# Kernel optimization log

Hardware: AMD Instinct MI355X
Metric: run time of the kernel (lower is better)

The kernel has to match this reference:

```python
import jax, jax.numpy as jnp
import numpy as np

L = 256            # model length (match states)
Q = 2 * L + 3      # num_states = 2*length + 3
M = 1              # num_models
B = 256            # batch of sequences
T = 512            # sequence length (timesteps)
EPS = 1e-16


def setup_inputs() -> dict:
    key = jax.random.key(0)
    k1, k2, k3 = jax.random.split(key, 3)
    return {
        "emission_probs": jax.random.uniform(k1, (T, M, B, Q), dtype=jnp.float32),
        "log_A": jax.random.normal(k2, (M, Q, Q), dtype=jnp.float32),
        "init_logits": jax.random.normal(k3, (M, Q), dtype=jnp.float32),
    }


def reference(emission_probs, log_A, init_logits):
    # Dense transition matrix per model (row-stochastic), as in transitioner.make_log_A()
    A = jax.nn.softmax(log_A, axis=-1)                 # (M, Q, Q)
    init_dist = jax.nn.softmax(init_logits, axis=-1)   # (M, Q)

    def norm_step(E, R, ll):
        # One scaled-forward update: multiply emission, normalize, accumulate loglik.
        E = jnp.maximum(E, EPS)
        R = jnp.maximum(R, EPS)
        a = E * R                                      # (M, B, Q)
        S = jnp.sum(a, axis=-1, keepdims=True)         # (M, B, 1)
        ll = ll + jnp.log(S)
        a = a / S
        return a, ll

    # t = 0: init=True -> R is the initial distribution (no transition applied)
    R0 = jnp.broadcast_to(init_dist[:, None, :], (M, B, Q))
    fwd0, ll0 = norm_step(emission_probs[0], R0, jnp.zeros((M, B, 1), jnp.float32))
    out0 = jnp.concatenate([jnp.log(fwd0), ll0], axis=-1)  # (M, B, Q+1)

    def step(carry, E_t):
        fwd, ll = carry
        # transitioner(old_scaled_forward): dense transition matvec per model
        R = jnp.einsum('mbq,mqk->mbk', fwd, A)
        a, ll = norm_step(E_t, R, ll)
        return (a, ll), jnp.concatenate([jnp.log(a), ll], axis=-1)

    _, outs = jax.lax.scan(step, (fwd0, ll0), emission_probs[1:])
    outs = jnp.concatenate([out0[None], outs], axis=0)     # (T, M, B, Q+1)
    # RNN output layout: (M*B, T, Q+1)
    return jnp.transpose(outs, (1, 2, 0, 3)).reshape(M * B, T, Q + 1)
```

## Files before the change

kernel.cpp:

```cpp
#include <hip/hip_runtime.h>
#include <cstdint>

typedef unsigned u32t;
typedef unsigned long long u64;
typedef float f32x4 __attribute__((ext_vector_type(4)));
typedef short s16x4 __attribute__((ext_vector_type(4)));

#define Qn   515
#define QP   520
#define Bn   256
#define Tn   512
#define OQ   516
#define EPSc 1e-16f
#define NSL  65
#define NT   5
#define KT   33
#define KTA  17
#define USTR 532
#define NGRP 32
#define NBLK 8
#define RWORDS 264

#define WS_AMATH 0
#define WS_INIT  565760
#define WS_PAY   568320
#define WS_FLG   (WS_PAY + 540672)
#define WS_TOTAL (WS_FLG + 32768)

#define L_FRAG 0
#define L_UST  (NT*KT*64*8)
#define L_USL  (L_UST + 16*USTR*2)
#define L_SIG  (L_USL + 8*68*4)
#define LDS_TOTAL (L_SIG + 128)

__device__ __forceinline__ unsigned bfbits(float x) {
    unsigned u = __builtin_bit_cast(unsigned, x);
    unsigned r = u + 0x7FFFu + ((u >> 16) & 1u);
    return r >> 16;
}
__device__ __forceinline__ float bflo(u32t w) {
    return __builtin_bit_cast(float, w << 16);
}
__device__ __forceinline__ float bfhi(u32t w) {
    return __builtin_bit_cast(float, w & 0xffff0000u);
}

__global__ void prep_A(const float* __restrict__ logA, unsigned* __restrict__ AMATh) {
    __shared__ float red[4];
    __shared__ float srow[Qn];
    int row = blockIdx.x, tid = threadIdx.x;
    if (row >= Qn) {
        for (int c = tid; c < 260; c += 256) AMATh[(size_t)row*260 + c] = 0u;
        return;
    }
    float mx = -1e30f;
    for (int c = tid; c < Qn; c += 256) { float x = logA[(size_t)row*Qn + c]; srow[c] = x; mx = fmaxf(mx, x); }
#pragma unroll
    for (int o = 32; o > 0; o >>= 1) mx = fmaxf(mx, __shfl_xor(mx, o));
    if ((tid & 63) == 0) red[tid >> 6] = mx;
    __syncthreads();
    mx = fmaxf(fmaxf(red[0], red[1]), fmaxf(red[2], red[3]));
    __syncthreads();
    float sm = 0.f;
    for (int c = tid; c < Qn; c += 256) sm += __expf(srow[c] - mx);
#pragma unroll
    for (int o = 32; o > 0; o >>= 1) sm += __shfl_xor(sm, o);
    if ((tid & 63) == 0) red[tid >> 6] = sm;
    __syncthreads();
    float inv = 1.f / (red[0] + red[1] + red[2] + red[3]);
    for (int c2 = tid; c2 < 260; c2 += 256) {
        int c = 2*c2;
        float v0 = (c   < Qn) ? __expf(srow[c]   - mx) * inv : 0.f;
        float v1 = (c+1 < Qn) ? __expf(srow[c+1] - mx) * inv : 0.f;
        AMATh[(size_t)row*260 + c2] = bfbits(v0) | (bfbits(v1) << 16);
    }
}

__global__ void prep_init(const float* __restrict__ il, float* __restrict__ INITD) {
    __shared__ float red[4];
    __shared__ float srow[Qn];
    int tid = threadIdx.x;
    float mx = -1e30f;
    for (int c = tid; c < Qn; c += 256) { float x = il[c]; srow[c] = x; mx = fmaxf(mx, x); }
#pragma unroll
    for (int o = 32; o > 0; o >>= 1) mx = fmaxf(mx, __shfl_xor(mx, o));
    if ((tid & 63) == 0) red[tid >> 6] = mx;
    __syncthreads();
    mx = fmaxf(fmaxf(red[0], red[1]), fmaxf(red[2], red[3]));
    __syncthreads();
    float sm = 0.f;
    for (int c = tid; c < Qn; c += 256) sm += __expf(srow[c] - mx);
#pragma unroll
    for (int o = 32; o > 0; o >>= 1) sm += __shfl_xor(sm, o);
    if ((tid & 63) == 0) red[tid >> 6] = sm;
    __syncthreads();
    float inv = 1.f / (red[0] + red[1] + red[2] + red[3]);
    for (int c = tid; c < 520; c += 256)
        INITD[c] = (c < Qn) ? __expf(srow[c] - mx) * inv : 0.f;
}

__global__ void __launch_bounds__(256, 1)
hmm_fwd(const float* __restrict__ E, const unsigned* __restrict__ AMATh,
        const float* __restrict__ INITD, float* __restrict__ out,
        u32t* __restrict__ pay, u32t* __restrict__ flg)
{
    extern __shared__ char smem[];
    uint2* frag = (uint2*)(smem + L_FRAG);
    unsigned short* ustage = (unsigned short*)(smem + L_UST);
    u32t* ustage32 = (u32t*)ustage;
    float* usl  = (float*)(smem + L_USL);
    float* invs = (float*)(smem + L_SIG);
    float* lsig = invs + 8;

    const int tid  = threadIdx.x;
    const int lane = tid & 63;
    const int wv   = tid >> 6;
    const int bid  = blockIdx.x;
    const int g    = bid & 31;
    const int j    = bid >> 5;
    const int b0   = g * 8;
    const int q0   = j * NSL;

    for (int f = tid; f < NT*KT*64; f += 256) {
        int tile = f >> 6, l = f & 63;
        int nt = tile / KT, kt = tile - nt*KT;
        int col = q0 + nt*16 + (l & 15);
        int kb  = kt*16 + ((l >> 4) << 2);
        unsigned h[4];
#pragma unroll
        for (int i = 0; i < 4; ++i) {
            int pk_ = kb + i;
            int jr = pk_ / 66, rr = pk_ - jr*66;
            unsigned hv = 0;
            if (rr < 65 && col < QP) {
                int qrow = jr*65 + rr;
                unsigned w = AMATh[(size_t)qrow*260 + (col >> 1)];
                hv = (col & 1) ? (w >> 16) : (w & 0xffffu);
            }
            h[i] = hv;
        }
        uint2 pk;
        pk.x = h[0] | (h[1] << 16);
        pk.y = h[2] | (h[3] << 16);
        frag[f] = pk;
    }
    for (int i = tid; i < 16*(USTR/2); i += 256) ustage32[i] = 0u;
    __syncthreads();

    const int ntn = (wv == 0) ? 2 : 1;
    const int nts0 = wv;
    int eoff[2][4];
#pragma unroll
    for (int sl = 0; sl < 2; ++sl) {
#pragma unroll
        for (int r = 0; r < 4; ++r) {
            int nt  = sl ? 4 : nts0;
            int row = ((lane >> 4) << 2) + r;
            int col = nt*16 + (lane & 15);
            int q   = q0 + col;
            bool ok = (lane < 32) && (col < NSL) && (q < Qn) && (sl < ntn);
            eoff[sl][r] = ok ? ((b0 + row)*Qn + q) : -1;
        }
    }
    const int rrow = tid >> 5;
    const int t32  = tid & 31;
    const int nw   = (t32 < 8) ? 9 : 8;

    float llreg = 0.f;
    float lsr = 0.f;
    u32t w9[9];

    auto pay_base = [&](int slot) { return pay + ((size_t)slot*NGRP + g)*(8*RWORDS); };
    auto flg_idx  = [&](int slot, int jj) { return ((unsigned)(slot*NGRP + g)*NBLK + jj)*16; };

    auto publish = [&](int s) {
        __syncthreads();
        u32t* pb = pay_base(s & 1);
        for (int p = tid; p < 8*33; p += 256) {
            int row = p / 33, c2 = p - row*33;
            float a0 = usl[row*68 + 2*c2];
            float a1 = usl[row*68 + 2*c2 + 1];
            u32t pk = bfbits(a0) | (bfbits(a1) << 16);
            __hip_atomic_store(&pb[row*RWORDS + 33*j + c2], pk,
                               __ATOMIC_RELAXED, __HIP_MEMORY_SCOPE_AGENT);
        }
        __syncthreads();
        if (tid == 0)
            __hip_atomic_store(&flg[flg_idx(s & 1, j)], (u32t)(s + 1),
                               __ATOMIC_RELAXED, __HIP_MEMORY_SCOPE_AGENT);
    };

    auto poll_flags = [&](int s) {
        const u32t* fb = flg + flg_idx((s - 1) & 1, 0);
        unsigned want = (unsigned)s;
        while (true) {
            u32t fv = 0xffffffffu;
            if (lane < 8)
                fv = __hip_atomic_load(&fb[lane*16], __ATOMIC_RELAXED, __HIP_MEMORY_SCOPE_AGENT);
            if (__all(fv >= want)) break;
        }
    };

    auto bulk_reduce = [&](int s) {
        const u32t* pb = pay_base((s - 1) & 1) + (size_t)rrow*RWORDS;
#pragma unroll
        for (int k = 0; k < 8; ++k)
            w9[k] = __hip_atomic_load(&pb[t32 + 32*k], __ATOMIC_RELAXED, __HIP_MEMORY_SCOPE_AGENT);
        w9[8] = (t32 < 8) ? __hip_atomic_load(&pb[256 + t32], __ATOMIC_RELAXED, __HIP_MEMORY_SCOPE_AGENT) : 0u;
        float sum = 0.f;
#pragma unroll
        for (int k = 0; k < 9; ++k) {
            if (k < nw) { sum += bflo(w9[k]) + bfhi(w9[k]); }
        }
#pragma unroll
        for (int o = 1; o < 32; o <<= 1) sum += __shfl_xor(sum, o);
        lsr = __logf(sum);
        llreg += lsr;
        if (t32 == 0) { invs[rrow] = 1.f / sum; lsig[rrow] = lsr; }
    };

    auto stage = [&]() {
        float iv = invs[rrow];
#pragma unroll
        for (int k = 0; k < 9; ++k) {
            if (k < nw) {
                int wi = (k < 8) ? (t32 + 32*k) : (256 + t32);
                u32t pk = bfbits(bflo(w9[k]) * iv) | (bfbits(bfhi(w9[k]) * iv) << 16);
                ustage32[rrow*(USTR/2) + wi] = pk;
            }
        }
    };

    auto emit_outputs = [&](int tOut) {
        if (t32 == 0 && j == 0)
            out[((size_t)(b0 + rrow)*Tn + tOut)*OQ + Qn] = llreg;
        float* orow = out + ((size_t)(b0 + rrow)*Tn + tOut)*OQ;
#pragma unroll
        for (int k = 0; k < 9; ++k) {
            if (k < nw) {
                int wi = (k < 8) ? (t32 + 32*k) : (256 + t32);
                int c0 = 2*wi;
#pragma unroll
                for (int h = 0; h < 2; ++h) {
                    int c = c0 + h;
                    int jr = c / 66, loc = c - jr*66;
                    if (jr == j && loc < 65) {
                        int q = q0 + loc;
                        if (q < Qn) {
                            float f = h ? bfhi(w9[k]) : bflo(w9[k]);
                            orow[q] = __logf(f) - lsr;
                        }
                    }
                }
            }
        }
    };

    for (int p = tid; p < 8*66; p += 256) {
        int row = p / 66, c = p - row*66;
        int q = q0 + c;
        float uv = 0.f;
        if (c < 65 && q < Qn)
            uv = fmaxf(E[(size_t)(b0+row)*Qn + q], EPSc) * fmaxf(INITD[q], EPSc);
        usl[row*68 + c] = uv;
    }
    publish(0);

    for (int s = 1; s < Tn; ++s) {
        float ev[2][4];
        size_t ebase = (size_t)s * Bn * Qn;
#pragma unroll
        for (int sl = 0; sl < 2; ++sl)
#pragma unroll
            for (int r = 0; r < 4; ++r)
                ev[sl][r] = (eoff[sl][r] >= 0) ? E[ebase + eoff[sl][r]] : 0.f;

        poll_flags(s);
        bulk_reduce(s);
        __syncthreads();
        stage();
        __syncthreads();

        f32x4 a0a = {0.f,0.f,0.f,0.f}, a0b = {0.f,0.f,0.f,0.f};
        f32x4 a1a = {0.f,0.f,0.f,0.f}, a1b = {0.f,0.f,0.f,0.f};
        {
            const unsigned short* urow = ustage + (lane & 15)*USTR + ((lane >> 4) << 2);
            const uint2* f0 = frag + (size_t)(nts0*KT)*64 + lane;
            const uint2* f1 = frag + (size_t)(4*KT)*64 + lane;
#pragma unroll 2
            for (int kt = 0; kt < KTA; ++kt) {
                s16x4 af = __builtin_bit_cast(s16x4, *(const uint2*)(urow + kt*16));
                a0a = __builtin_amdgcn_mfma_f32_16x16x16bf16_1k(af, __builtin_bit_cast(s16x4, f0[kt*64]), a0a, 0, 0, 0);
                if (ntn == 2)
                    a1a = __builtin_amdgcn_mfma_f32_16x16x16bf16_1k(af, __builtin_bit_cast(s16x4, f1[kt*64]), a1a, 0, 0, 0);
                int k2 = kt + KTA;
                if (k2 < KT) {
                    s16x4 af2 = __builtin_bit_cast(s16x4, *(const uint2*)(urow + k2*16));
                    a0b = __builtin_amdgcn_mfma_f32_16x16x16bf16_1k(af2, __builtin_bit_cast(s16x4, f0[k2*64]), a0b, 0, 0, 0);
                    if (ntn == 2)
                        a1b = __builtin_amdgcn_mfma_f32_16x16x16bf16_1k(af2, __builtin_bit_cast(s16x4, f1[k2*64]), a1b, 0, 0, 0);
                }
            }
        }
        if (lane < 32) {
#pragma unroll
            for (int r = 0; r < 4; ++r) {
                int row = ((lane >> 4) << 2) + r;
                {
                    int col = nts0*16 + (lane & 15);
                    if (col < NSL) {
                        float R = fmaxf(a0a[r] + a0b[r], EPSc);
                        int q = q0 + col;
                        usl[row*68 + col] = (q < Qn) ? fmaxf(ev[0][r], EPSc) * R : 0.f;
                    }
                }
                if (ntn == 2) {
                    int col = 64 + (lane & 15);
                    if (col < NSL) {
                        float R = fmaxf(a1a[r] + a1b[r], EPSc);
                        int q = q0 + col;
                        usl[row*68 + col] = (q < Qn) ? fmaxf(ev[1][r], EPSc) * R : 0.f;
                    }
                }
            }
        }
        publish(s);

        emit_outputs(s - 1);
    }

    poll_flags(Tn);
    bulk_reduce(Tn);
    emit_outputs(Tn - 1);
}

extern "C" void kernel_launch(void* const* d_in, const int* in_sizes, int n_in,
                              void* d_out, int out_size, void* d_ws, size_t ws_size,
                              hipStream_t stream) {
    (void)in_sizes; (void)n_in; (void)out_size;
    if (ws_size < (size_t)WS_TOTAL) return;

    const float* E    = (const float*)d_in[0];
    const float* logA = (const float*)d_in[1];
    const float* il   = (const float*)d_in[2];
    float* out = (float*)d_out;
    char*  ws  = (char*)d_ws;

    unsigned* AMATh = (unsigned*)(ws + WS_AMATH);
    float*    INITD = (float*)(ws + WS_INIT);
    u32t*     pay   = (u32t*)(ws + WS_PAY);
    u32t*     flgp  = (u32t*)(ws + WS_FLG);

    hipMemsetAsync(ws + WS_FLG, 0, 32768, stream);

    prep_A<<<544, 256, 0, stream>>>(logA, AMATh);
    prep_init<<<1, 256, 0, stream>>>(il, INITD);

    static_assert(LDS_TOTAL < 160*1024, "LDS budget");
    hipFuncSetAttribute(reinterpret_cast<const void*>(hmm_fwd),
                        hipFuncAttributeMaxDynamicSharedMemorySize, LDS_TOTAL);
    hmm_fwd<<<256, 256, LDS_TOTAL, stream>>>(E, AMATh, INITD, out, pay, flgp);
}
```

Before: 3.090 ms.

## Use tagged payload words and XCC-aware group assignment for inter-block exchange

Replaces the separate payload-then-flag handshake with 64-bit words that pack the bf16 data together with a step tag, so consumers poll the data directly and two block-wide barriers per publish are dropped. Blocks read their XCC id and are assigned to batch groups so that all 8 blocks of a group sit on the same XCC where possible. Intra-XCC traffic then uses sc0 (L2-coherent) loads and stores, and cross-XCC groups use sc1. A panic flag escalates a group to sc1 if polling stalls. This aims to cut per-step synchronisation latency, at the cost of doubled payload bytes and a fragile reliance on cache-scope semantics and co-residency.

New measurement: 4.318 ms. +39.7%, slower.

```diff
diff --git a/kernel.cpp b/kernel.cpp
--- a/kernel.cpp
+++ b/kernel.cpp
@@ -19,31 +19,27 @@
 #define USTR 532
 #define NGRP 32
 #define NBLK 8
-#define RWORDS 264
+#define RW   264
 
 #define WS_AMATH 0
 #define WS_INIT  565760
-#define WS_PAY   568320
-#define WS_FLG   (WS_PAY + 540672)
-#define WS_TOTAL (WS_FLG + 32768)
+#define WS_FBUF  568320
+#define WS_CNT   (WS_FBUF + 1081344)
+#define WS_PAN   (WS_CNT + 256)
+#define WS_TOTAL (WS_PAN + 2048)
 
 #define L_FRAG 0
 #define L_UST  (NT*KT*64*8)
 #define L_USL  (L_UST + 16*USTR*2)
-#define L_SIG  (L_USL + 8*68*4)
-#define LDS_TOTAL (L_SIG + 128)
+#define LDS_TOTAL (L_USL + 8*68*4 + 64)
 
 __device__ __forceinline__ unsigned bfbits(float x) {
     unsigned u = __builtin_bit_cast(unsigned, x);
     unsigned r = u + 0x7FFFu + ((u >> 16) & 1u);
     return r >> 16;
 }
-__device__ __forceinline__ float bflo(u32t w) {
-    return __builtin_bit_cast(float, w << 16);
-}
-__device__ __forceinline__ float bfhi(u32t w) {
-    return __builtin_bit_cast(float, w & 0xffff0000u);
-}
+__device__ __forceinline__ float bflo(u32t w) { return __builtin_bit_cast(float, w << 16); }
+__device__ __forceinline__ float bfhi(u32t w) { return __builtin_bit_cast(float, w & 0xffff0000u); }
 
 __global__ void prep_A(const float* __restrict__ logA, unsigned* __restrict__ AMATh) {
     __shared__ float red[4];
@@ -102,24 +98,63 @@
 __global__ void __launch_bounds__(256, 1)
 hmm_fwd(const float* __restrict__ E, const unsigned* __restrict__ AMATh,
         const float* __restrict__ INITD, float* __restrict__ out,
-        u32t* __restrict__ pay, u32t* __restrict__ flg)
+        u64* __restrict__ fbuf, unsigned* __restrict__ cnt,
+        unsigned* __restrict__ pan)
 {
     extern __shared__ char smem[];
     uint2* frag = (uint2*)(smem + L_FRAG);
     unsigned short* ustage = (unsigned short*)(smem + L_UST);
     u32t* ustage32 = (u32t*)ustage;
-    float* usl  = (float*)(smem + L_USL);
-    float* invs = (float*)(smem + L_SIG);
-    float* lsig = invs + 8;
+    float* usl = (float*)(smem + L_USL);
+    const u64* uslq = (const u64*)usl;
+    __shared__ unsigned sh_reg[10];
 
     const int tid  = threadIdx.x;
     const int lane = tid & 63;
     const int wv   = tid >> 6;
-    const int bid  = blockIdx.x;
-    const int g    = bid & 31;
-    const int j    = bid >> 5;
-    const int b0   = g * 8;
-    const int q0   = j * NSL;
+
+    if (tid == 0) {
+        unsigned xcc;
+        asm volatile("s_getreg_b32 %0, hwreg(HW_REG_XCC_ID)" : "=s"(xcc));
+        xcc &= 7u;
+        unsigned k = __hip_atomic_fetch_add(&cnt[xcc], 1u, __ATOMIC_RELAXED, __HIP_MEMORY_SCOPE_AGENT);
+        unsigned n[8];
+        while (true) {
+            unsigned tot = 0;
+#pragma unroll
+            for (int y = 0; y < 8; ++y) {
+                n[y] = __hip_atomic_load(&cnt[y], __ATOMIC_RELAXED, __HIP_MEMORY_SCOPE_AGENT);
+                tot += n[y];
+            }
+            if (tot == 256u) break;
+            __builtin_amdgcn_s_sleep(8);
+        }
+        sh_reg[0] = xcc; sh_reg[1] = k;
+#pragma unroll
+        for (int y = 0; y < 8; ++y) sh_reg[2+y] = n[y];
+    }
+    __syncthreads();
+
+    int g, j;
+    bool esc;
+    {
+        unsigned x = sh_reg[0], kk = sh_reg[1];
+        unsigned fgx = 0, basex = 0, totalfull = 0, lbefore = 0;
+#pragma unroll
+        for (unsigned y = 0; y < 8; ++y) {
+            unsigned ny = sh_reg[2+y], f = ny >> 3;
+            if (y < x) { basex += f; lbefore += ny - (f << 3); }
+            if (y == x) fgx = f;
+            totalfull += f;
+        }
+        if (kk < (fgx << 3)) { g = (int)(basex + (kk >> 3)); j = (int)(kk & 7u); esc = false; }
+        else {
+            unsigned L = lbefore + (kk - (fgx << 3));
+            g = (int)(totalfull + (L >> 3)); j = (int)(L & 7u); esc = true;
+        }
+    }
+    const int b0  = g * 8;
+    const int q0  = j * NSL;
 
     for (int f = tid; f < NT*KT*64; f += 256) {
         int tile = f >> 6, l = f & 63;
@@ -145,7 +180,6 @@
         frag[f] = pk;
     }
     for (int i = tid; i < 16*(USTR/2); i += 256) ustage32[i] = 0u;
-    __syncthreads();
 
     const int ntn = (wv == 0) ? 2 : 1;
     const int nts0 = wv;
@@ -166,67 +200,88 @@
     const int t32  = tid & 31;
     const int nw   = (t32 < 8) ? 9 : 8;
 
-    float llreg = 0.f;
-    float lsr = 0.f;
-    u32t w9[9];
-
-    auto pay_base = [&](int slot) { return pay + ((size_t)slot*NGRP + g)*(8*RWORDS); };
-    auto flg_idx  = [&](int slot, int jj) { return ((unsigned)(slot*NGRP + g)*NBLK + jj)*16; };
+    float llreg = 0.f, lsr = 0.f;
+    u64 w9[9];
 
     auto publish = [&](int s) {
-        __syncthreads();
-        u32t* pb = pay_base(s & 1);
+        u64 tagw = ((u64)(unsigned)(s + 1)) << 32;
+        u64* fw = fbuf + ((size_t)(s & 1)*NGRP + g)*(8*RW);
         for (int p = tid; p < 8*33; p += 256) {
             int row = p / 33, c2 = p - row*33;
-            float a0 = usl[row*68 + 2*c2];
-            float a1 = usl[row*68 + 2*c2 + 1];
-            u32t pk = bfbits(a0) | (bfbits(a1) << 16);
-            __hip_atomic_store(&pb[row*RWORDS + 33*j + c2], pk,
-                               __ATOMIC_RELAXED, __HIP_MEMORY_SCOPE_AGENT);
-        }
-        __syncthreads();
-        if (tid == 0)
-            __hip_atomic_store(&flg[flg_idx(s & 1, j)], (u32t)(s + 1),
-                               __ATOMIC_RELAXED, __HIP_MEMORY_SCOPE_AGENT);
+            u64 uv = uslq[row*34 + c2];
+            float a0 = __builtin_bit_cast(float, (unsigned)uv);
+            float a1 = __builtin_bit_cast(float, (unsigned)(uv >> 32));
+            u64 word = (u64)(bfbits(a0) | (bfbits(a1) << 16)) | tagw;
+            u64* ap = fw + (size_t)row*RW + j*33 + c2;
+            if (esc) asm volatile("global_store_dwordx2 %0, %1, off sc1" :: "v"(ap), "v"(word) : "memory");
+            else     asm volatile("global_store_dwordx2 %0, %1, off sc0" :: "v"(ap), "v"(word) : "memory");
+        }
     };
 
-    auto poll_flags = [&](int s) {
-        const u32t* fb = flg + flg_idx((s - 1) & 1, 0);
-        unsigned want = (unsigned)s;
-        while (true) {
-            u32t fv = 0xffffffffu;
-            if (lane < 8)
-                fv = __hip_atomic_load(&fb[lane*16], __ATOMIC_RELAXED, __HIP_MEMORY_SCOPE_AGENT);
-            if (__all(fv >= want)) break;
-        }
-    };
-
-    auto bulk_reduce = [&](int s) {
-        const u32t* pb = pay_base((s - 1) & 1) + (size_t)rrow*RWORDS;
-#pragma unroll
-        for (int k = 0; k < 8; ++k)
-            w9[k] = __hip_atomic_load(&pb[t32 + 32*k], __ATOMIC_RELAXED, __HIP_MEMORY_SCOPE_AGENT);
-        w9[8] = (t32 < 8) ? __hip_atomic_load(&pb[256 + t32], __ATOMIC_RELAXED, __HIP_MEMORY_SCOPE_AGENT) : 0u;
+    auto poll_read = [&](int s) -> float {
+        const unsigned want = (unsigned)s;
+        const u64* pb = fbuf + (((size_t)((s-1) & 1)*NGRP + g)*8 + rrow)*RW;
+        unsigned pend = (t32 < 8) ? 0x1FFu : 0xFFu;
+        unsigned it = 0;
+        while (pend) {
+#pragma unroll
+            for (int k = 0; k < 9; ++k) if (pend & (1u << k)) {
+                const u64* ap = pb + ((k < 8) ? (t32 + 32*k) : (256 + t32));
+                if (esc) asm volatile("global_load_dwordx2 %0, %1, off sc1" : "=v"(w9[k]) : "v"(ap));
+                else     asm volatile("global_load_dwordx2 %0, %1, off sc0" : "=v"(w9[k]) : "v"(ap));
+            }
+            asm volatile("s_waitcnt vmcnt(0)" ::: "memory");
+            __builtin_amdgcn_sched_barrier(0);
+#pragma unroll
+            for (int k = 0; k < 9; ++k)
+                if ((pend & (1u << k)) && (unsigned)(w9[k] >> 32) == want) pend &= ~(1u << k);
+            ++it;
+            if (!esc && pend && (it & 63u) == 0u) {
+                const unsigned* pp = pan + (unsigned)g*16;
+                unsigned pv;
+                asm volatile("global_load_dword %0, %1, off sc1" : "=v"(pv) : "v"(pp));
+                asm volatile("s_waitcnt vmcnt(0)" ::: "memory");
+                __builtin_amdgcn_sched_barrier(0);
+                if (!pv && it >= 2048u) {
+                    unsigned one = 1u;
+                    asm volatile("global_store_dword %0, %1, off sc1" :: "v"(pp), "v"(one) : "memory");
+                    pv = 1u;
+                }
+                if (pv) {
+                    esc = true;
+                    u64 tagw = ((u64)want) << 32;
+                    u64* fw = fbuf + ((size_t)((s-1) & 1)*NGRP + g)*(8*RW);
+                    for (int p = tid; p < 8*33; p += 256) {
+                        int row = p / 33, c2 = p - row*33;
+                        u64 uv = uslq[row*34 + c2];
+                        float a0 = __builtin_bit_cast(float, (unsigned)uv);
+                        float a1 = __builtin_bit_cast(float, (unsigned)(uv >> 32));
+                        u64 word = (u64)(bfbits(a0) | (bfbits(a1) << 16)) | tagw;
+                        u64* ap = fw + (size_t)row*RW + j*33 + c2;
+                        asm volatile("global_store_dwordx2 %0, %1, off sc1" :: "v"(ap), "v"(word) : "memory");
+                    }
+                }
+            }
+        }
         float sum = 0.f;
 #pragma unroll
         for (int k = 0; k < 9; ++k) {
-            if (k < nw) { sum += bflo(w9[k]) + bfhi(w9[k]); }
+            if (k < nw) { u32t pr = (u32t)w9[k]; sum += bflo(pr) + bfhi(pr); }
         }
 #pragma unroll
         for (int o = 1; o < 32; o <<= 1) sum += __shfl_xor(sum, o);
         lsr = __logf(sum);
         llreg += lsr;
-        if (t32 == 0) { invs[rrow] = 1.f / sum; lsig[rrow] = lsr; }
+        return 1.f / sum;
     };
 
-    auto stage = [&]() {
-        float iv = invs[rrow];
+    auto stage = [&](float iv) {
 #pragma unroll
         for (int k = 0; k < 9; ++k) {
             if (k < nw) {
                 int wi = (k < 8) ? (t32 + 32*k) : (256 + t32);
-                u32t pk = bfbits(bflo(w9[k]) * iv) | (bfbits(bfhi(w9[k]) * iv) << 16);
-                ustage32[rrow*(USTR/2) + wi] = pk;
+                u32t pr = (u32t)w9[k];
+                ustage32[rrow*(USTR/2) + wi] = bfbits(bflo(pr)*iv) | (bfbits(bfhi(pr)*iv) << 16);
             }
         }
     };
@@ -239,6 +294,7 @@
         for (int k = 0; k < 9; ++k) {
             if (k < nw) {
                 int wi = (k < 8) ? (t32 + 32*k) : (256 + t32);
+                u32t pr = (u32t)w9[k];
                 int c0 = 2*wi;
 #pragma unroll
                 for (int h = 0; h < 2; ++h) {
@@ -247,7 +303,7 @@
                     if (jr == j && loc < 65) {
                         int q = q0 + loc;
                         if (q < Qn) {
-                            float f = h ? bfhi(w9[k]) : bflo(w9[k]);
+                            float f = h ? bfhi(pr) : bflo(pr);
                             orow[q] = __logf(f) - lsr;
                         }
                     }
@@ -264,6 +320,7 @@
             uv = fmaxf(E[(size_t)(b0+row)*Qn + q], EPSc) * fmaxf(INITD[q], EPSc);
         usl[row*68 + c] = uv;
     }
+    __syncthreads();
     publish(0);
 
     for (int s = 1; s < Tn; ++s) {
@@ -275,10 +332,8 @@
             for (int r = 0; r < 4; ++r)
                 ev[sl][r] = (eoff[sl][r] >= 0) ? E[ebase + eoff[sl][r]] : 0.f;
 
-        poll_flags(s);
-        bulk_reduce(s);
-        __syncthreads();
-        stage();
+        float iv = poll_read(s);
+        stage(iv);
         __syncthreads();
 
         f32x4 a0a = {0.f,0.f,0.f,0.f}, a0b = {0.f,0.f,0.f,0.f};
@@ -324,13 +379,12 @@
                 }
             }
         }
+        __syncthreads();
         publish(s);
-
         emit_outputs(s - 1);
     }
 
-    poll_flags(Tn);
-    bulk_reduce(Tn);
+    poll_read(Tn);
     emit_outputs(Tn - 1);
 }
 
@@ -348,10 +402,11 @@
 
     unsigned* AMATh = (unsigned*)(ws + WS_AMATH);
     float*    INITD = (float*)(ws + WS_INIT);
-    u32t*     pay   = (u32t*)(ws + WS_PAY);
-    u32t*     flgp  = (u32t*)(ws + WS_FLG);
-
-    hipMemsetAsync(ws + WS_FLG, 0, 32768, stream);
+    u64*      fbuf  = (u64*)(ws + WS_FBUF);
+    unsigned* cnt   = (unsigned*)(ws + WS_CNT);
+    unsigned* pan   = (unsigned*)(ws + WS_PAN);
+
+    hipMemsetAsync(ws + WS_FBUF, 0, WS_TOTAL - WS_FBUF, stream);
 
     prep_A<<<544, 256, 0, stream>>>(logA, AMATh);
     prep_init<<<1, 256, 0, stream>>>(il, INITD);
@@ -359,5 +414,5 @@
     static_assert(LDS_TOTAL < 160*1024, "LDS budget");
     hipFuncSetAttribute(reinterpret_cast<const void*>(hmm_fwd),
                         hipFuncAttributeMaxDynamicSharedMemorySize, LDS_TOTAL);
-    hmm_fwd<<<256, 256, LDS_TOTAL, stream>>>(E, AMATh, INITD, out, pay, flgp);
+    hmm_fwd<<<256, 256, LDS_TOTAL, stream>>>(E, AMATh, INITD, out, fbuf, cnt, pan);
 }
```
